# Optimization experiments

Hardware: AMD Instinct MI355X
Metric: run time of the kernel (lower is better)

The kernel has to match this reference:

```python
import jax, jax.numpy as jnp
import numpy as np

B, T, H, DK, DV, HID, C = 2, 4096, 16, 128, 128, 2048, 64  # chunk size 64 (fla default)
EPS = 1e-5


def setup_inputs() -> dict:
    key = jax.random.key(0)
    ks = jax.random.split(key, 8)
    s = 0.02
    return dict(
        hidden_ab=jax.random.normal(ks[0], (B, T, HID), jnp.float32),
        hidden_g=jax.random.normal(ks[1], (B, T, HID), jnp.float32),
        q=jax.random.normal(ks[2], (B, T, H, DK), jnp.float32),
        k=jax.random.normal(ks[3], (B, T, H, DK), jnp.float32),
        v=jax.random.normal(ks[4], (B, T, H, DV), jnp.float32),
        Wb=jax.random.normal(ks[5], (HID, H), jnp.float32) * s,
        Wg=jax.random.normal(ks[6], (HID, H), jnp.float32) * s,
        o_norm_w=jnp.ones((DV,), jnp.float32),
        o_proj_w=jax.random.normal(ks[7], (H, DV, DK), jnp.float32) * s,
    )


def _l2norm(x):
    return x * jax.lax.rsqrt(jnp.sum(x * x, -1, keepdims=True) + 1e-6)


def reference(hidden_ab, hidden_g, q, k, v, Wb, Wg, o_norm_w, o_proj_w):
    # beta gate per head (training path: sigmoid(b_proj(hidden_ab)))
    beta = jax.nn.sigmoid(hidden_ab @ Wb)  # [B,T,H]
    # qk_norm == 'l2' -> l2 normalization inside the kernel, q scaled by dk^-0.5
    q = _l2norm(q)
    k = _l2norm(k)
    scale = DK ** -0.5
    N = T // C

    def toc(x, d):  # [B,T,H,d] -> [N,B,H,C,d]
        return x.reshape(B, N, C, H, d).transpose(1, 0, 3, 2, 4)

    qc = toc(q * scale, DK)
    kc = toc(k, DK)
    vc = toc(v, DV)
    bc = beta.reshape(B, N, C, H).transpose(1, 0, 3, 2)  # [N,B,H,C]

    k_beta = kc * bc[..., None]
    v_beta = vc * bc[..., None]

    # intra-chunk UT transform: Tm = (I + strict_lower(k_beta k^T))^{-1}
    Lm = jnp.tril(jnp.einsum('nbhik,nbhjk->nbhij', k_beta, kc), -1)  # [N,B,H,C,C]
    eye = jnp.eye(C, dtype=q.dtype)
    Tm = jax.scipy.linalg.solve_triangular(eye + Lm, jnp.broadcast_to(eye, Lm.shape), lower=True)
    u = Tm @ v_beta   # [N,B,H,C,DV]
    w = Tm @ k_beta   # [N,B,H,C,DK]
    attn = jnp.tril(jnp.einsum('nbhik,nbhjk->nbhij', qc, kc))  # causal intra-chunk scores

    def step(S, ins):  # S: [B,H,DK,DV] carried state
        qn, kn, an, un, wn = ins
        vi = un - wn @ S                                   # corrected values
        on = qn @ S + an @ vi                              # inter + intra chunk output
        S = S + jnp.einsum('bhck,bhcv->bhkv', kn, vi)      # state update
        return S, on

    S0 = jnp.zeros((B, H, DK, DV), q.dtype)
    _, o = jax.lax.scan(step, S0, (qc, kc, attn, u, w))    # o: [N,B,H,C,DV]
    o = o.transpose(1, 0, 3, 2, 4).reshape(B, T, H, DV)

    # FusedRMSNormSwishGate with per-head scalar gate broadcast over DV
    g = hidden_g @ Wg  # [B,T,H]
    o = o * jax.lax.rsqrt(jnp.mean(o * o, -1, keepdims=True) + EPS) * o_norm_w
    o = o * (g * jax.nn.sigmoid(g))[..., None]

    # GroupLinear: per-head DV -> head_dim projection, then flatten heads
    out = jnp.einsum('bthv,hvd->bthd', o, o_proj_w).reshape(B, T, H * DK)
    return out
```

## Files before the change

kernel.cpp:

```cpp
#include <hip/hip_runtime.h>
#include <hip/hip_bf16.h>

#define BB 2
#define TT 4096
#define HH 16
#define DKk 128
#define DVv 128
#define HIDD 2048
#define CC 64
#define NN 64
#define GG 8
#define QSCALE 0.08838834764831845f

static __device__ __forceinline__ unsigned short f2bf(float f) {
  unsigned u = __float_as_uint(f);
  u += 0x7fffu + ((u >> 16) & 1u);
  return (unsigned short)(u >> 16);
}
static __device__ __forceinline__ float bf2f(unsigned short s) {
  return __uint_as_float(((unsigned)s) << 16);
}

static __device__ __forceinline__ void barrier_lds_only() {
  asm volatile("s_waitcnt lgkmcnt(0)\n\ts_barrier" ::: "memory");
}

typedef short bf8 __attribute__((ext_vector_type(8)));
typedef float f4 __attribute__((ext_vector_type(4)));

__global__ __launch_bounds__(256) void k0_wt(
    const float* __restrict__ Wb, const float* __restrict__ Wg,
    unsigned short* __restrict__ Wtb, unsigned short* __restrict__ Wtg) {
  int blk = blockIdx.x;
  const float* W = (blk < 8) ? Wb : Wg;
  unsigned short* Wt = (blk < 8) ? Wtb : Wtg;
  int k0 = (blk & 7) * 256;
  int tid = threadIdx.x;
  __shared__ unsigned short st[16][272];
  const float* p = W + (size_t)(k0 + tid) * HH;
#pragma unroll
  for (int h4 = 0; h4 < 4; h4++) {
    float4 x = *(const float4*)(p + h4 * 4);
    st[h4 * 4 + 0][tid] = f2bf(x.x);
    st[h4 * 4 + 1][tid] = f2bf(x.y);
    st[h4 * 4 + 2][tid] = f2bf(x.z);
    st[h4 * 4 + 3][tid] = f2bf(x.w);
  }
  __syncthreads();
  int h = tid >> 4, c = (tid & 15) << 4;
#pragma unroll
  for (int j = 0; j < 16; j++)
    Wt[(size_t)h * HIDD + k0 + c + j] = st[h][c + j];
}

__global__ __launch_bounds__(256) void k0p_pt(
    const float* __restrict__ opw, unsigned short* __restrict__ Ppt) {
  int h = blockIdx.x;
  int tid = threadIdx.x;
  __shared__ unsigned short sp[128 * 132];
  const float* P = opw + (size_t)h * (DVv * DKk);
  for (int it = 0; it < 16; it++) {
    int idx = it * 256 + tid;
    int vv = idx >> 5, d4 = (idx & 31) << 2;
    float4 x = *(const float4*)(P + vv * 128 + d4);
    sp[vv * 132 + d4 + 0] = f2bf(x.x);
    sp[vv * 132 + d4 + 1] = f2bf(x.y);
    sp[vv * 132 + d4 + 2] = f2bf(x.z);
    sp[vv * 132 + d4 + 3] = f2bf(x.w);
  }
  __syncthreads();
  unsigned short* dst = Ppt + (size_t)h * (DVv * DKk);
  for (int it = 0; it < 8; it++) {
    int idx = it * 256 + tid;
    int d = idx >> 4, v8 = (idx & 15) << 3;
    unsigned short tmp[8];
#pragma unroll
    for (int j = 0; j < 8; j++) tmp[j] = sp[(v8 + j) * 132 + d];
    *(uint4*)&dst[d * 128 + v8] = *(uint4*)tmp;
  }
}

__global__ __launch_bounds__(256) void k1_beta_g(
    const float* __restrict__ hab, const float* __restrict__ hg,
    const unsigned short* __restrict__ Wtb, const unsigned short* __restrict__ Wtg,
    float* __restrict__ beta, float* __restrict__ graw) {
  int tile = blockIdx.x;
  int tid = threadIdx.x;
  int w = tid >> 6, lane = tid & 63;
  int proj = w >> 1, ks = w & 1;
  int n16 = lane & 15, qd = lane >> 4;
  const float* hid = proj ? hg : hab;
  const unsigned short* Wt = proj ? Wtg : Wtb;
  size_t rowbase = (size_t)(tile * 16 + n16) * HIDD;
  int k0 = ks * 1024;

  f4 acc = {0.f, 0.f, 0.f, 0.f};
  for (int s = 0; s < 32; s++) {
    int kk = k0 + s * 32 + qd * 8;
    const float* hp = hid + rowbase + kk;
    float4 h0 = *(const float4*)hp;
    float4 h1 = *(const float4*)(hp + 4);
    bf8 a;
    a[0] = (short)f2bf(h0.x); a[1] = (short)f2bf(h0.y);
    a[2] = (short)f2bf(h0.z); a[3] = (short)f2bf(h0.w);
    a[4] = (short)f2bf(h1.x); a[5] = (short)f2bf(h1.y);
    a[6] = (short)f2bf(h1.z); a[7] = (short)f2bf(h1.w);
    bf8 b = *(const bf8*)&Wt[(size_t)n16 * HIDD + kk];
    acc = __builtin_amdgcn_mfma_f32_16x16x32_bf16(a, b, acc, 0, 0, 0);
  }

  __shared__ float red[2][16][17];
  if (ks == 1) {
#pragma unroll
    for (int r = 0; r < 4; r++) red[proj][qd * 4 + r][n16] = acc[r];
  }
  __syncthreads();
  if (ks == 0) {
#pragma unroll
    for (int r = 0; r < 4; r++) {
      float s = acc[r] + red[proj][qd * 4 + r][n16];
      size_t t = (size_t)(tile * 16 + qd * 4 + r) * HH + n16;
      if (proj == 0) beta[t] = 1.f / (1.f + expf(-s));
      else           graw[t] = s;
    }
  }
}

__global__ __launch_bounds__(256) void k2_l2norm(
    const float* __restrict__ q, const float* __restrict__ k,
    unsigned short* __restrict__ qn, unsigned short* __restrict__ kn) {
  int lane = threadIdx.x & 63, wave = threadIdx.x >> 6;
  for (int u = 0; u < 2; u++) {
    int vec = blockIdx.x * 8 + wave * 2 + u;
    size_t off = (size_t)vec * 64 + lane;
    float2 q2 = ((const float2*)q)[off];
    float2 k2 = ((const float2*)k)[off];
    float sq = q2.x * q2.x + q2.y * q2.y;
    float sk = k2.x * k2.x + k2.y * k2.y;
#pragma unroll
    for (int m = 32; m; m >>= 1) { sq += __shfl_xor(sq, m); sk += __shfl_xor(sk, m); }
    float rq = rsqrtf(sq + 1e-6f) * QSCALE;
    float rk = rsqrtf(sk + 1e-6f);
    unsigned pq = (unsigned)f2bf(q2.x * rq) | ((unsigned)f2bf(q2.y * rq) << 16);
    unsigned pk = (unsigned)f2bf(k2.x * rk) | ((unsigned)f2bf(k2.y * rk) << 16);
    ((unsigned*)qn)[off] = pq;
    ((unsigned*)kn)[off] = pk;
  }
}

#define SW 72
#define K3_M0R 8704
#define K3_M0T 13312
#define K3_M1R 17920
#define K3_M1T 22528
#define K3_TB  27136
#define K3_ARENA 31744

__global__ __launch_bounds__(256) void k3_chunk(
    const unsigned short* __restrict__ qn, const unsigned short* __restrict__ kn,
    const float* __restrict__ beta,
    unsigned short* __restrict__ ATg, unsigned short* __restrict__ Ktg) {
  int cid = blockIdx.x;
  int n = cid & (NN - 1);
  int bh = cid / NN;
  int h = bh & (HH - 1);
  int b = bh / HH;
  int tid = threadIdx.x;
  int w = tid >> 6;
  int lane = tid & 63;
  int n16 = lane & 15;
  int qd = lane >> 4;
  int r0 = w * 16;

  __shared__ __align__(16) unsigned short arena[K3_ARENA];
  __shared__ float sb[CC];
  unsigned short* sk = arena;
  unsigned short* sq = arena + 8704;

  int t0 = n * CC;
#pragma unroll
  for (int p = 0; p < 4; p++) {
    int id = p * 256 + tid, row = id >> 4, c8 = (id & 15) << 3;
    size_t g = ((size_t)((b * TT + t0 + row) * HH + h)) * DKk + c8;
    *(uint4*)&sk[row * 136 + c8] = *(const uint4*)(kn + g);
    *(uint4*)&sq[row * 136 + c8] = *(const uint4*)(qn + g);
  }
  if (tid < CC) sb[tid] = beta[(size_t)((b * TT + t0 + tid) * HH + h)];
  __syncthreads();

  f4 at[4], mk[4];
#pragma unroll
  for (int ct = 0; ct < 4; ct++) { at[ct] = (f4){0,0,0,0}; mk[ct] = (f4){0,0,0,0}; }
#pragma unroll
  for (int s = 0; s < 4; s++) {
    bf8 aq = *(const bf8*)&sq[(r0 + n16) * 136 + s * 32 + qd * 8];
    bf8 ak = *(const bf8*)&sk[(r0 + n16) * 136 + s * 32 + qd * 8];
#pragma unroll
    for (int ct = 0; ct < 4; ct++) {
      bf8 bk = *(const bf8*)&sk[(ct * 16 + n16) * 136 + s * 32 + qd * 8];
      at[ct] = __builtin_amdgcn_mfma_f32_16x16x32_bf16(aq, bk, at[ct], 0, 0, 0);
      mk[ct] = __builtin_amdgcn_mfma_f32_16x16x32_bf16(ak, bk, mk[ct], 0, 0, 0);
    }
  }

  f4 tf[4];
  float mpv[4][4];
#pragma unroll
  for (int ct = 0; ct < 4; ct++) {
#pragma unroll
    for (int r = 0; r < 4; r++) {
      int i = r0 + qd * 4 + r, j = ct * 16 + n16;
      at[ct][r] = (j <= i) ? at[ct][r] : 0.f;
      float mp = (j < i) ? -sb[i] * mk[ct][r] : 0.f;
      mpv[ct][r] = mp;
      tf[ct][r] = (i == j) ? 1.f : mp;
    }
  }
  __syncthreads();

#pragma unroll
  for (int ct = 0; ct < 4; ct++) {
#pragma unroll
    for (int r = 0; r < 4; r++) {
      int i = r0 + qd * 4 + r, j = ct * 16 + n16;
      unsigned short hm = f2bf(mpv[ct][r]);
      arena[K3_M0R + i * SW + j] = hm;
      arena[K3_M0T + j * SW + i] = hm;
      arena[K3_TB + j * SW + i] = f2bf(tf[ct][r]);
    }
  }
  __syncthreads();

  int p = 0;
  for (int it = 1; it <= 5; it++) {
    int mrp = p ? K3_M1R : K3_M0R, mtp = p ? K3_M1T : K3_M0T;
    int mrn = p ? K3_M0R : K3_M1R, mtn = p ? K3_M0T : K3_M1T;
    f4 nr[4];
#pragma unroll
    for (int ct = 0; ct < 4; ct++) nr[ct] = (f4){0,0,0,0};
#pragma unroll
    for (int s = 0; s < 2; s++) {
      bf8 a = *(const bf8*)&arena[mrp + (r0 + n16) * SW + s * 32 + qd * 8];
#pragma unroll
      for (int ct = 0; ct < 4; ct++) {
        bf8 bb = *(const bf8*)&arena[mtp + (ct * 16 + n16) * SW + s * 32 + qd * 8];
        nr[ct] = __builtin_amdgcn_mfma_f32_16x16x32_bf16(a, bb, nr[ct], 0, 0, 0);
      }
    }
#pragma unroll
    for (int ct = 0; ct < 4; ct++) {
#pragma unroll
      for (int r = 0; r < 4; r++) {
        int i = r0 + qd * 4 + r, j = ct * 16 + n16;
        unsigned short hm = f2bf(nr[ct][r]);
        arena[mrn + i * SW + j] = hm;
        arena[mtn + j * SW + i] = hm;
      }
    }
    __syncthreads();

#pragma unroll
    for (int s = 0; s < 2; s++) {
      bf8 a = *(const bf8*)&arena[mrn + (r0 + n16) * SW + s * 32 + qd * 8];
#pragma unroll
      for (int ct = 0; ct < 4; ct++) {
        bf8 bb = *(const bf8*)&arena[K3_TB + (ct * 16 + n16) * SW + s * 32 + qd * 8];
        tf[ct] = __builtin_amdgcn_mfma_f32_16x16x32_bf16(a, bb, tf[ct], 0, 0, 0);
      }
    }
    __syncthreads();

    if (it < 5) {
#pragma unroll
      for (int ct = 0; ct < 4; ct++) {
#pragma unroll
        for (int r = 0; r < 4; r++) {
          int i = r0 + qd * 4 + r, j = ct * 16 + n16;
          arena[K3_TB + j * SW + i] = f2bf(tf[ct][r]);
        }
      }
    }
    p = 1 - p;
  }

#pragma unroll
  for (int ct = 0; ct < 4; ct++) {
#pragma unroll
    for (int r = 0; r < 4; r++) {
      int i = r0 + qd * 4 + r, j = ct * 16 + n16;
      arena[K3_M0R + i * SW + j] = f2bf(at[ct][r]);
      arena[K3_TB + j * SW + i] = f2bf(tf[ct][r]);
    }
  }
  __syncthreads();

  {
    f4 ac[4];
#pragma unroll
    for (int ct = 0; ct < 4; ct++) ac[ct] = (f4){0,0,0,0};
#pragma unroll
    for (int s = 0; s < 2; s++) {
      bf8 a = *(const bf8*)&arena[K3_M0R + (r0 + n16) * SW + s * 32 + qd * 8];
#pragma unroll
      for (int ct = 0; ct < 4; ct++) {
        bf8 bb = *(const bf8*)&arena[K3_TB + (ct * 16 + n16) * SW + s * 32 + qd * 8];
        ac[ct] = __builtin_amdgcn_mfma_f32_16x16x32_bf16(a, bb, ac[ct], 0, 0, 0);
      }
    }
    size_t abase = (size_t)cid * (CC * CC);
#pragma unroll
    for (int ct = 0; ct < 4; ct++)
#pragma unroll
      for (int r = 0; r < 4; r++)
        ATg[abase + (r0 + qd * 4 + r) * CC + ct * 16 + n16] = f2bf(ac[ct][r]);
  }

  {
    size_t kbase = (size_t)cid * (DKk * CC);
#pragma unroll
    for (int t = 0; t < 2; t++) {
      int dkt = w * 32 + t * 16;
      f4 ac[4];
#pragma unroll
      for (int ct = 0; ct < 4; ct++) ac[ct] = (f4){0,0,0,0};
#pragma unroll
      for (int s = 0; s < 2; s++) {
        bf8 a;
#pragma unroll
        for (int jj = 0; jj < 8; jj++)
          a[jj] = (short)sk[(s * 32 + qd * 8 + jj) * 136 + dkt + n16];
#pragma unroll
        for (int ct = 0; ct < 4; ct++) {
          bf8 bb = *(const bf8*)&arena[K3_TB + (ct * 16 + n16) * SW + s * 32 + qd * 8];
          ac[ct] = __builtin_amdgcn_mfma_f32_16x16x32_bf16(a, bb, ac[ct], 0, 0, 0);
        }
      }
#pragma unroll
      for (int ct = 0; ct < 4; ct++)
#pragma unroll
        for (int r = 0; r < 4; r++)
          Ktg[kbase + (dkt + qd * 4 + r) * CC + ct * 16 + n16] = f2bf(ac[ct][r]);
    }
  }
}

struct K4Frag {
  bf8 k0, k1, k2, k3;
  bf8 q0, q1, q2, q3;
  bf8 a0, a1;
  bf8 t0, t1, t2, t3;
  float4 vv;
  float b0, b1, b2, b3;
};

static __device__ __forceinline__ void k4_prefetch(
    K4Frag& F, int n,
    const unsigned short* knb, const unsigned short* qnb,
    const unsigned short* atb, const unsigned short* ktb,
    const float* vb, const float* bb) {
  const unsigned short* kp = knb + (size_t)n * (CC * HH * DKk);
  F.k0 = *(const bf8*)(kp);
  F.k1 = *(const bf8*)(kp + 32);
  F.k2 = *(const bf8*)(kp + 64);
  F.k3 = *(const bf8*)(kp + 96);
  const unsigned short* qp = qnb + (size_t)n * (CC * HH * DKk);
  F.q0 = *(const bf8*)(qp);
  F.q1 = *(const bf8*)(qp + 32);
  F.q2 = *(const bf8*)(qp + 64);
  F.q3 = *(const bf8*)(qp + 96);
  const unsigned short* ap = atb + (size_t)n * (CC * CC);
  F.a0 = *(const bf8*)(ap);
  F.a1 = *(const bf8*)(ap + 32);
  const unsigned short* tp = ktb + (size_t)n * (DKk * CC);
  F.t0 = *(const bf8*)(tp);
  F.t1 = *(const bf8*)(tp + 32);
  F.t2 = *(const bf8*)(tp + 1024);
  F.t3 = *(const bf8*)(tp + 1024 + 32);
  F.vv = *(const float4*)(vb + (size_t)n * (CC * HH * DVv));
  const float* bp = bb + (size_t)n * (CC * HH);
  F.b0 = bp[0]; F.b1 = bp[HH]; F.b2 = bp[2 * HH]; F.b3 = bp[3 * HH];
}

static __device__ __forceinline__ void k4_body(
    const K4Frag& F, K4Frag& FN, int n, bool pf,
    f4& S0, f4& S1,
    unsigned short* xT, unsigned short* sSb,
    float* opn,
    int n16, int qd, int r0, int dkbase,
    const unsigned short* knb, const unsigned short* qnb,
    const unsigned short* atb, const unsigned short* ktb,
    const float* vb, const float* bb) {
  if (pf) k4_prefetch(FN, n + 1, knb, qnb, atb, ktb, vb, bb);

  {
    int col = r0 + n16;
    xT[(qd * 4 + 0) * SW + col] = f2bf(F.vv.x);
    xT[(qd * 4 + 1) * SW + col] = f2bf(F.vv.y);
    xT[(qd * 4 + 2) * SW + col] = f2bf(F.vv.z);
    xT[(qd * 4 + 3) * SW + col] = f2bf(F.vv.w);
  }
  barrier_lds_only();

  f4 oacc;
  {
    bf8 bS0 = *(const bf8*)&sSb[n16 * 136 + 0 + qd * 8];
    bf8 bS1 = *(const bf8*)&sSb[n16 * 136 + 32 + qd * 8];
    bf8 bS2 = *(const bf8*)&sSb[n16 * 136 + 64 + qd * 8];
    bf8 bS3 = *(const bf8*)&sSb[n16 * 136 + 96 + qd * 8];
    f4 xa = {0.f, 0.f, 0.f, 0.f}, xc = {0.f, 0.f, 0.f, 0.f};
    f4 oa = {0.f, 0.f, 0.f, 0.f}, ob = {0.f, 0.f, 0.f, 0.f};
    xa = __builtin_amdgcn_mfma_f32_16x16x32_bf16(F.k0, bS0, xa, 0, 0, 0);
    xa = __builtin_amdgcn_mfma_f32_16x16x32_bf16(F.k1, bS1, xa, 0, 0, 0);
    xc = __builtin_amdgcn_mfma_f32_16x16x32_bf16(F.k2, bS2, xc, 0, 0, 0);
    xc = __builtin_amdgcn_mfma_f32_16x16x32_bf16(F.k3, bS3, xc, 0, 0, 0);
    oa = __builtin_amdgcn_mfma_f32_16x16x32_bf16(F.q0, bS0, oa, 0, 0, 0);
    oa = __builtin_amdgcn_mfma_f32_16x16x32_bf16(F.q1, bS1, oa, 0, 0, 0);
    ob = __builtin_amdgcn_mfma_f32_16x16x32_bf16(F.q2, bS2, ob, 0, 0, 0);
    ob = __builtin_amdgcn_mfma_f32_16x16x32_bf16(F.q3, bS3, ob, 0, 0, 0);
    oacc = oa + ob;
    float bv[4] = {F.b0, F.b1, F.b2, F.b3};
#pragma unroll
    for (int r = 0; r < 4; r++) {
      int c = r0 + qd * 4 + r;
      float vval = bf2f(xT[n16 * SW + c]);
      xT[n16 * SW + c] = f2bf(bv[r] * (vval - (xa[r] + xc[r])));
    }
  }
  barrier_lds_only();

  {
    bf8 bx0 = *(const bf8*)&xT[n16 * SW + qd * 8];
    bf8 bx1 = *(const bf8*)&xT[n16 * SW + 32 + qd * 8];
    oacc = __builtin_amdgcn_mfma_f32_16x16x32_bf16(F.a0, bx0, oacc, 0, 0, 0);
    oacc = __builtin_amdgcn_mfma_f32_16x16x32_bf16(F.a1, bx1, oacc, 0, 0, 0);
#pragma unroll
    for (int r = 0; r < 4; r++) opn[r * (HH * DVv)] = oacc[r];
    S0 = __builtin_amdgcn_mfma_f32_16x16x32_bf16(F.t0, bx0, S0, 0, 0, 0);
    S0 = __builtin_amdgcn_mfma_f32_16x16x32_bf16(F.t1, bx1, S0, 0, 0, 0);
    S1 = __builtin_amdgcn_mfma_f32_16x16x32_bf16(F.t2, bx0, S1, 0, 0, 0);
    S1 = __builtin_amdgcn_mfma_f32_16x16x32_bf16(F.t3, bx1, S1, 0, 0, 0);
    uint2 w0, w1;
    w0.x = (unsigned)f2bf(S0[0]) | ((unsigned)f2bf(S0[1]) << 16);
    w0.y = (unsigned)f2bf(S0[2]) | ((unsigned)f2bf(S0[3]) << 16);
    w1.x = (unsigned)f2bf(S1[0]) | ((unsigned)f2bf(S1[1]) << 16);
    w1.y = (unsigned)f2bf(S1[2]) | ((unsigned)f2bf(S1[3]) << 16);
    *(uint2*)&sSb[n16 * 136 + dkbase + qd * 4] = w0;
    *(uint2*)&sSb[n16 * 136 + dkbase + 16 + qd * 4] = w1;
  }
}

__global__ __launch_bounds__(256, 1) void k4_scan(
    const unsigned short* __restrict__ qn, const unsigned short* __restrict__ kn,
    const float* __restrict__ v, const float* __restrict__ beta,
    const unsigned short* __restrict__ ATg, const unsigned short* __restrict__ Ktg,
    float* __restrict__ o) {
  int bi = blockIdx.x;
  int jg = bi >> 5;
  int bh = bi & 31;
  int h = bh & (HH - 1);
  int b = bh >> 4;
  int tid = threadIdx.x;
  int j0 = jg * 16;
  int w = tid >> 6;
  int lane = tid & 63;
  int n16 = lane & 15;
  int qd = lane >> 4;
  int r0 = w * 16;
  int dkbase = w * 32;

  __shared__ __align__(16) unsigned short sSb[16 * 136];
  __shared__ __align__(16) unsigned short sxT[2][16 * SW];

  f4 S0 = {0.f, 0.f, 0.f, 0.f}, S1 = {0.f, 0.f, 0.f, 0.f};
  for (int i = tid; i < 16 * 136; i += 256) sSb[i] = 0;

  const unsigned short* knb =
      kn + ((size_t)((b * TT + r0 + n16) * HH + h)) * DKk + qd * 8;
  const unsigned short* qnb =
      qn + ((size_t)((b * TT + r0 + n16) * HH + h)) * DKk + qd * 8;
  size_t bhN = (size_t)(b * HH + h) * NN;
  const unsigned short* atb = ATg + bhN * (CC * CC) + (r0 + n16) * 64 + qd * 8;
  const unsigned short* ktb = Ktg + bhN * (DKk * CC) + (dkbase + n16) * 64 + qd * 8;
  const float* vb =
      v + ((size_t)((b * TT + r0 + n16) * HH + h)) * DVv + j0 + qd * 4;
  const float* bb = beta + (size_t)((b * TT + r0 + qd * 4) * HH + h);
  float* opb =
      o + ((size_t)((b * TT + r0 + qd * 4) * HH + h)) * DVv + j0 + n16;

  K4Frag FA, FB;
  k4_prefetch(FA, 0, knb, qnb, atb, ktb, vb, bb);

  for (int n = 0; n < NN; n += 2) {
    k4_body(FA, FB, n, true, S0, S1, sxT[0], sSb,
            opb + (size_t)n * (CC * HH * DVv),
            n16, qd, r0, dkbase, knb, qnb, atb, ktb, vb, bb);
    k4_body(FB, FA, n + 1, n + 2 < NN, S0, S1, sxT[1], sSb,
            opb + (size_t)(n + 1) * (CC * HH * DVv),
            n16, qd, r0, dkbase, knb, qnb, atb, ktb, vb, bb);
  }
}

__global__ __launch_bounds__(256) void k5_out(
    const float* __restrict__ graw, const float* __restrict__ onw,
    const unsigned short* __restrict__ Ppt, float* __restrict__ out) {
  int bi = blockIdx.x;
  int h = bi & (HH - 1);
  int tt = (bi >> 4) & 127;
  int b = bi >> 11;
  int t0 = tt * 32;
  int tid = threadIdx.x;
  int w = tid >> 6;
  int lane = tid & 63;
  int n16 = lane & 15;
  int qd = lane >> 4;

  __shared__ __align__(16) float so[32 * 132];
  __shared__ float smul[32];
  __shared__ float snw[DVv];

  for (int r = 0; r < 16; r++) {
    int idx = r * 256 + tid;
    int t = idx >> 7, d = idx & 127;
    so[t * 132 + d] = out[((size_t)((b * TT + t0 + t) * HH + h)) * DVv + d];
  }
  if (tid < DVv) snw[tid] = onw[tid];
  __syncthreads();

  {
    int t = tid >> 3, l8 = tid & 7;
    float ss = 0.f;
    for (int j = 0; j < 16; j++) { float x = so[t * 132 + l8 + (j << 3)]; ss += x * x; }
    ss += __shfl_down(ss, 4, 8);
    ss += __shfl_down(ss, 2, 8);
    ss += __shfl_down(ss, 1, 8);
    if (l8 == 0) {
      float rms = rsqrtf(ss * (1.f / 128.f) + 1e-5f);
      float gv = graw[(size_t)((b * TT + t0 + t) * HH + h)];
      float sig = 1.f / (1.f + expf(-gv));
      smul[t] = rms * gv * sig;
    }
  }
  __syncthreads();
  for (int r = 0; r < 16; r++) {
    int idx = r * 256 + tid;
    int t = idx >> 7, d = idx & 127;
    so[t * 132 + d] *= smul[t] * snw[d];
  }
  __syncthreads();

  {
    const unsigned short* Pb = Ppt + (size_t)h * (DVv * DKk);
    int dt0 = w * 2;
#pragma unroll
    for (int m = 0; m < 2; m++) {
      bf8 A[4];
#pragma unroll
      for (int ks = 0; ks < 4; ks++) {
        const float* sp = &so[(m * 16 + n16) * 132 + ks * 32 + qd * 8];
        float4 f0 = *(const float4*)sp;
        float4 f1 = *(const float4*)(sp + 4);
        A[ks][0] = (short)f2bf(f0.x); A[ks][1] = (short)f2bf(f0.y);
        A[ks][2] = (short)f2bf(f0.z); A[ks][3] = (short)f2bf(f0.w);
        A[ks][4] = (short)f2bf(f1.x); A[ks][5] = (short)f2bf(f1.y);
        A[ks][6] = (short)f2bf(f1.z); A[ks][7] = (short)f2bf(f1.w);
      }
#pragma unroll
      for (int dti = 0; dti < 2; dti++) {
        int dt = dt0 + dti;
        f4 acc = {0.f, 0.f, 0.f, 0.f};
#pragma unroll
        for (int ks = 0; ks < 4; ks++) {
          bf8 Bf = *(const bf8*)(Pb + (dt * 16 + n16) * 128 + ks * 32 + qd * 8);
          acc = __builtin_amdgcn_mfma_f32_16x16x32_bf16(A[ks], Bf, acc, 0, 0, 0);
        }
#pragma unroll
        for (int r = 0; r < 4; r++) {
          size_t go = ((size_t)(b * TT + t0 + m * 16 + qd * 4 + r)) * (HH * DKk)
                      + h * DKk + dt * 16 + n16;
          out[go] = acc[r];
        }
      }
    }
  }
}

extern "C" void kernel_launch(void* const* d_in, const int* in_sizes, int n_in,
                              void* d_out, int out_size, void* d_ws, size_t ws_size,
                              hipStream_t stream) {
  (void)in_sizes; (void)n_in; (void)out_size; (void)ws_size;
  const float* hab = (const float*)d_in[0];
  const float* hg  = (const float*)d_in[1];
  const float* q   = (const float*)d_in[2];
  const float* k   = (const float*)d_in[3];
  const float* v   = (const float*)d_in[4];
  const float* Wb  = (const float*)d_in[5];
  const float* Wg  = (const float*)d_in[6];
  const float* onw = (const float*)d_in[7];
  const float* opw = (const float*)d_in[8];
  float* out = (float*)d_out;

  char* ws = (char*)d_ws;
  float* beta          = (float*)(ws);
  float* graw          = (float*)(ws + 524288);
  unsigned short* qn   = (unsigned short*)(ws + 1048576);
  unsigned short* kn   = (unsigned short*)(ws + 34603008);
  unsigned short* ATg  = (unsigned short*)(ws + 68157440);
  unsigned short* Ktg  = (unsigned short*)(ws + 84934656);
  unsigned short* Wtb  = (unsigned short*)(ws + 118489088);
  unsigned short* Wtg  = (unsigned short*)(ws + 118554624);
  unsigned short* Ppt  = (unsigned short*)(ws + 118620160);

  hipLaunchKernelGGL(k0_wt, dim3(16), dim3(256), 0, stream,
                     Wb, Wg, Wtb, Wtg);
  hipLaunchKernelGGL(k0p_pt, dim3(HH), dim3(256), 0, stream,
                     opw, Ppt);
  hipLaunchKernelGGL(k1_beta_g, dim3(TT * BB / 16), dim3(256), 0, stream,
                     hab, hg, Wtb, Wtg, beta, graw);
  hipLaunchKernelGGL(k2_l2norm, dim3(BB * TT * HH / 8), dim3(256), 0, stream,
                     q, k, qn, kn);
  hipLaunchKernelGGL(k3_chunk, dim3(BB * HH * NN), dim3(256), 0, stream,
                     qn, kn, beta, ATg, Ktg);
  hipLaunchKernelGGL(k4_scan, dim3(BB * HH * GG), dim3(256), 0, stream,
                     qn, kn, v, beta, ATg, Ktg, out);
  hipLaunchKernelGGL(k5_out, dim3(BB * (TT / 32) * HH), dim3(256), 0, stream,
                     graw, onw, Ppt, out);
}
```

Measured before the change: 533.6 us.

## Restructure scan: precompute beta-scaled k and v, double-buffer state to drop a barrier

Two new precomputed inputs feed the sequential scan. A beta-scaled bf16 key is written alongside qn/kn, and a new kernel writes beta-scaled, transposed bf16 values that reuse the kn buffer once k3 has finished with it. The scan stages the shared beta-k tile in double-buffered LDS and double-buffers the state, so each chunk step needs one barrier instead of two, and it uses packed bf16 conversion instructions. The cost is an extra pre-pass kernel, more global traffic and more LDS, with ordering that depends on k3 finishing before vt overwrites kn.

```diff
diff --git a/kernel.cpp b/kernel.cpp
--- a/kernel.cpp
+++ b/kernel.cpp
@@ -20,13 +20,26 @@
 static __device__ __forceinline__ float bf2f(unsigned short s) {
   return __uint_as_float(((unsigned)s) << 16);
 }
+static __device__ __forceinline__ unsigned cvtpk(float lo, float hi) {
+  unsigned r;
+  asm("v_cvt_pk_bf16_f32 %0, %1, %2" : "=v"(r) : "v"(lo), "v"(hi));
+  return r;
+}
 
 static __device__ __forceinline__ void barrier_lds_only() {
   asm volatile("s_waitcnt lgkmcnt(0)\n\ts_barrier" ::: "memory");
 }
 
 typedef short bf8 __attribute__((ext_vector_type(8)));
+typedef short bf4 __attribute__((ext_vector_type(4)));
 typedef float f4 __attribute__((ext_vector_type(4)));
+
+static __device__ __forceinline__ bf4 pack_bf4(float a, float b, float c, float d) {
+  union { uint2 u; bf4 s; } t;
+  t.u.x = cvtpk(a, b);
+  t.u.y = cvtpk(c, d);
+  return t.s;
+}
 
 __global__ __launch_bounds__(256) void k0_wt(
     const float* __restrict__ Wb, const float* __restrict__ Wg,
@@ -128,23 +141,68 @@
 
 __global__ __launch_bounds__(256) void k2_l2norm(
     const float* __restrict__ q, const float* __restrict__ k,
-    unsigned short* __restrict__ qn, unsigned short* __restrict__ kn) {
+    const float* __restrict__ beta,
+    unsigned short* __restrict__ qn, unsigned short* __restrict__ kn,
+    unsigned short* __restrict__ kb) {
   int lane = threadIdx.x & 63, wave = threadIdx.x >> 6;
   for (int u = 0; u < 2; u++) {
     int vec = blockIdx.x * 8 + wave * 2 + u;
     size_t off = (size_t)vec * 64 + lane;
     float2 q2 = ((const float2*)q)[off];
     float2 k2 = ((const float2*)k)[off];
+    float bv = beta[vec];
     float sq = q2.x * q2.x + q2.y * q2.y;
     float sk = k2.x * k2.x + k2.y * k2.y;
 #pragma unroll
     for (int m = 32; m; m >>= 1) { sq += __shfl_xor(sq, m); sk += __shfl_xor(sk, m); }
     float rq = rsqrtf(sq + 1e-6f) * QSCALE;
     float rk = rsqrtf(sk + 1e-6f);
+    float rkb = rk * bv;
     unsigned pq = (unsigned)f2bf(q2.x * rq) | ((unsigned)f2bf(q2.y * rq) << 16);
     unsigned pk = (unsigned)f2bf(k2.x * rk) | ((unsigned)f2bf(k2.y * rk) << 16);
+    unsigned pb = (unsigned)f2bf(k2.x * rkb) | ((unsigned)f2bf(k2.y * rkb) << 16);
     ((unsigned*)qn)[off] = pq;
     ((unsigned*)kn)[off] = pk;
+    ((unsigned*)kb)[off] = pb;
+  }
+}
+
+__global__ __launch_bounds__(256) void k2v_vt(
+    const float* __restrict__ v, const float* __restrict__ beta,
+    unsigned short* __restrict__ vt) {
+  int bi = blockIdx.x;
+  int n = bi & (NN - 1);
+  int bh = bi >> 6;
+  int h = bh & (HH - 1);
+  int b = bh >> 4;
+  int tid = threadIdx.x;
+  int t0 = n * CC;
+
+  __shared__ float sov[64 * 132];
+  __shared__ float sbv[64];
+
+  for (int p = 0; p < 8; p++) {
+    int idx = p * 256 + tid;
+    int row = idx >> 5, d4 = (idx & 31) << 2;
+    float4 x = *(const float4*)(v + ((size_t)((b * TT + t0 + row) * HH + h)) * DVv + d4);
+    *(float4*)&sov[row * 132 + d4] = x;
+  }
+  if (tid < 64) sbv[tid] = beta[(size_t)((b * TT + t0 + tid) * HH + h)];
+  __syncthreads();
+
+  unsigned short* dst = vt + (size_t)(bh * NN + n) * 8192;
+  for (int p = 0; p < 8; p++) {
+    int q = p * 256 + tid;
+    int rt = q >> 9, col = (q >> 2) & 127, i4 = q & 3;
+    int m = rt * 16 + i4 * 4;
+    float x0 = sbv[m + 0] * sov[(m + 0) * 132 + col];
+    float x1 = sbv[m + 1] * sov[(m + 1) * 132 + col];
+    float x2 = sbv[m + 2] * sov[(m + 2) * 132 + col];
+    float x3 = sbv[m + 3] * sov[(m + 3) * 132 + col];
+    uint2 wv;
+    wv.x = cvtpk(x0, x1);
+    wv.y = cvtpk(x2, x3);
+    *(uint2*)&dst[(size_t)q * 4] = wv;
   }
 }
 
@@ -344,25 +402,17 @@
   }
 }
 
-struct K4Frag {
-  bf8 k0, k1, k2, k3;
+struct K4F {
   bf8 q0, q1, q2, q3;
   bf8 a0, a1;
   bf8 t0, t1, t2, t3;
-  float4 vv;
-  float b0, b1, b2, b3;
+  uint2 v0, v1, v2, v3;
 };
 
-static __device__ __forceinline__ void k4_prefetch(
-    K4Frag& F, int n,
-    const unsigned short* knb, const unsigned short* qnb,
-    const unsigned short* atb, const unsigned short* ktb,
-    const float* vb, const float* bb) {
-  const unsigned short* kp = knb + (size_t)n * (CC * HH * DKk);
-  F.k0 = *(const bf8*)(kp);
-  F.k1 = *(const bf8*)(kp + 32);
-  F.k2 = *(const bf8*)(kp + 64);
-  F.k3 = *(const bf8*)(kp + 96);
+static __device__ __forceinline__ void k4_pref(
+    K4F& F, int n,
+    const unsigned short* qnb, const unsigned short* atb,
+    const unsigned short* ktb, const unsigned short* vtb) {
   const unsigned short* qp = qnb + (size_t)n * (CC * HH * DKk);
   F.q0 = *(const bf8*)(qp);
   F.q1 = *(const bf8*)(qp + 32);
@@ -375,83 +425,102 @@
   F.t0 = *(const bf8*)(tp);
   F.t1 = *(const bf8*)(tp + 32);
   F.t2 = *(const bf8*)(tp + 1024);
-  F.t3 = *(const bf8*)(tp + 1024 + 32);
-  F.vv = *(const float4*)(vb + (size_t)n * (CC * HH * DVv));
-  const float* bp = bb + (size_t)n * (CC * HH);
-  F.b0 = bp[0]; F.b1 = bp[HH]; F.b2 = bp[2 * HH]; F.b3 = bp[3 * HH];
+  F.t3 = *(const bf8*)(tp + 1056);
+  const unsigned short* vp = vtb + (size_t)n * 8192;
+  F.v0 = *(const uint2*)(vp);
+  F.v1 = *(const uint2*)(vp + 2048);
+  F.v2 = *(const uint2*)(vp + 4096);
+  F.v3 = *(const uint2*)(vp + 6144);
 }
 
 static __device__ __forceinline__ void k4_body(
-    const K4Frag& F, K4Frag& FN, int n, bool pf,
-    f4& S0, f4& S1,
-    unsigned short* xT, unsigned short* sSb,
-    float* opn,
-    int n16, int qd, int r0, int dkbase,
-    const unsigned short* knb, const unsigned short* qnb,
-    const unsigned short* atb, const unsigned short* ktb,
-    const float* vb, const float* bb) {
-  if (pf) k4_prefetch(FN, n + 1, knb, qnb, atb, ktb, vb, bb);
-
+    const K4F& F, K4F& FN, int n,
+    f4& S0, f4& S1, uint4* KB,
+    const unsigned short* sSrd, unsigned short* sSwr,
+    const unsigned short* kbRd, unsigned short* kbWr,
+    unsigned short* xbw, float* opn,
+    int tid, int lane, int n16, int qd, int dkbase,
+    const unsigned short* qnb, const unsigned short* atb,
+    const unsigned short* ktb, const unsigned short* vtb,
+    const unsigned short* kbg, const size_t* gkb) {
+  if (n + 1 < NN) {
+#pragma unroll
+    for (int p = 0; p < 4; p++)
+      *(uint4*)&kbWr[(size_t)(p * 256 + tid) * 8] = KB[p];
+  }
+  if (n + 2 < NN) {
+#pragma unroll
+    for (int p = 0; p < 4; p++)
+      KB[p] = *(const uint4*)(kbg + gkb[p] + (size_t)(n + 2) * (CC * HH * DKk));
+  }
+  if (n + 1 < NN) k4_pref(FN, n + 1, qnb, atb, ktb, vtb);
+
+  bf8 bS0 = *(const bf8*)&sSrd[n16 * 136 + 0  + qd * 8];
+  bf8 bS1 = *(const bf8*)&sSrd[n16 * 136 + 32 + qd * 8];
+  bf8 bS2 = *(const bf8*)&sSrd[n16 * 136 + 64 + qd * 8];
+  bf8 bS3 = *(const bf8*)&sSrd[n16 * 136 + 96 + qd * 8];
+
+  f4 oa = {0.f, 0.f, 0.f, 0.f}, ob = {0.f, 0.f, 0.f, 0.f};
+  oa = __builtin_amdgcn_mfma_f32_16x16x32_bf16(F.q0, bS0, oa, 0, 0, 0);
+  oa = __builtin_amdgcn_mfma_f32_16x16x32_bf16(F.q1, bS1, oa, 0, 0, 0);
+  ob = __builtin_amdgcn_mfma_f32_16x16x32_bf16(F.q2, bS2, ob, 0, 0, 0);
+  ob = __builtin_amdgcn_mfma_f32_16x16x32_bf16(F.q3, bS3, ob, 0, 0, 0);
+
+  f4 xlo[4], xhi[4];
+#pragma unroll
+  for (int rt = 0; rt < 4; rt++) {
+    bf8 kf0 = *(const bf8*)&kbRd[(size_t)((rt * 4 + 0) * 64 + lane) * 8];
+    bf8 kf1 = *(const bf8*)&kbRd[(size_t)((rt * 4 + 1) * 64 + lane) * 8];
+    bf8 kf2 = *(const bf8*)&kbRd[(size_t)((rt * 4 + 2) * 64 + lane) * 8];
+    bf8 kf3 = *(const bf8*)&kbRd[(size_t)((rt * 4 + 3) * 64 + lane) * 8];
+    f4 lo = {0.f, 0.f, 0.f, 0.f}, hi = {0.f, 0.f, 0.f, 0.f};
+    lo = __builtin_amdgcn_mfma_f32_16x16x32_bf16(kf0, bS0, lo, 0, 0, 0);
+    lo = __builtin_amdgcn_mfma_f32_16x16x32_bf16(kf1, bS1, lo, 0, 0, 0);
+    hi = __builtin_amdgcn_mfma_f32_16x16x32_bf16(kf2, bS2, hi, 0, 0, 0);
+    hi = __builtin_amdgcn_mfma_f32_16x16x32_bf16(kf3, bS3, hi, 0, 0, 0);
+    xlo[rt] = lo;
+    xhi[rt] = hi;
+  }
   {
-    int col = r0 + n16;
-    xT[(qd * 4 + 0) * SW + col] = f2bf(F.vv.x);
-    xT[(qd * 4 + 1) * SW + col] = f2bf(F.vv.y);
-    xT[(qd * 4 + 2) * SW + col] = f2bf(F.vv.z);
-    xT[(qd * 4 + 3) * SW + col] = f2bf(F.vv.w);
-  }
+    const uint2 vv[4] = {F.v0, F.v1, F.v2, F.v3};
+#pragma unroll
+    for (int rt = 0; rt < 4; rt++) {
+      float w0 = bf2f((unsigned short)(vv[rt].x & 0xffffu));
+      float w1 = bf2f((unsigned short)(vv[rt].x >> 16));
+      float w2 = bf2f((unsigned short)(vv[rt].y & 0xffffu));
+      float w3 = bf2f((unsigned short)(vv[rt].y >> 16));
+      bf4 pw = pack_bf4(w0 - (xlo[rt][0] + xhi[rt][0]),
+                        w1 - (xlo[rt][1] + xhi[rt][1]),
+                        w2 - (xlo[rt][2] + xhi[rt][2]),
+                        w3 - (xlo[rt][3] + xhi[rt][3]));
+      *(bf4*)&xbw[n16 * 88 + rt * 16 + qd * 4] = pw;
+    }
+  }
+  bf8 bx0 = *(const bf8*)&xbw[n16 * 88 + 0  + qd * 8];
+  bf8 bx1 = *(const bf8*)&xbw[n16 * 88 + 32 + qd * 8];
+
+  f4 oacc = oa + ob;
+  oacc = __builtin_amdgcn_mfma_f32_16x16x32_bf16(F.a0, bx0, oacc, 0, 0, 0);
+  oacc = __builtin_amdgcn_mfma_f32_16x16x32_bf16(F.a1, bx1, oacc, 0, 0, 0);
+#pragma unroll
+  for (int r = 0; r < 4; r++) opn[r * (HH * DVv)] = oacc[r];
+
+  S0 = __builtin_amdgcn_mfma_f32_16x16x32_bf16(F.t0, bx0, S0, 0, 0, 0);
+  S0 = __builtin_amdgcn_mfma_f32_16x16x32_bf16(F.t1, bx1, S0, 0, 0, 0);
+  S1 = __builtin_amdgcn_mfma_f32_16x16x32_bf16(F.t2, bx0, S1, 0, 0, 0);
+  S1 = __builtin_amdgcn_mfma_f32_16x16x32_bf16(F.t3, bx1, S1, 0, 0, 0);
+
+  *(bf4*)&sSwr[n16 * 136 + dkbase + qd * 4] =
+      pack_bf4(S0[0], S0[1], S0[2], S0[3]);
+  *(bf4*)&sSwr[n16 * 136 + dkbase + 16 + qd * 4] =
+      pack_bf4(S1[0], S1[1], S1[2], S1[3]);
+
   barrier_lds_only();
-
-  f4 oacc;
-  {
-    bf8 bS0 = *(const bf8*)&sSb[n16 * 136 + 0 + qd * 8];
-    bf8 bS1 = *(const bf8*)&sSb[n16 * 136 + 32 + qd * 8];
-    bf8 bS2 = *(const bf8*)&sSb[n16 * 136 + 64 + qd * 8];
-    bf8 bS3 = *(const bf8*)&sSb[n16 * 136 + 96 + qd * 8];
-    f4 xa = {0.f, 0.f, 0.f, 0.f}, xc = {0.f, 0.f, 0.f, 0.f};
-    f4 oa = {0.f, 0.f, 0.f, 0.f}, ob = {0.f, 0.f, 0.f, 0.f};
-    xa = __builtin_amdgcn_mfma_f32_16x16x32_bf16(F.k0, bS0, xa, 0, 0, 0);
-    xa = __builtin_amdgcn_mfma_f32_16x16x32_bf16(F.k1, bS1, xa, 0, 0, 0);
-    xc = __builtin_amdgcn_mfma_f32_16x16x32_bf16(F.k2, bS2, xc, 0, 0, 0);
-    xc = __builtin_amdgcn_mfma_f32_16x16x32_bf16(F.k3, bS3, xc, 0, 0, 0);
-    oa = __builtin_amdgcn_mfma_f32_16x16x32_bf16(F.q0, bS0, oa, 0, 0, 0);
-    oa = __builtin_amdgcn_mfma_f32_16x16x32_bf16(F.q1, bS1, oa, 0, 0, 0);
-    ob = __builtin_amdgcn_mfma_f32_16x16x32_bf16(F.q2, bS2, ob, 0, 0, 0);
-    ob = __builtin_amdgcn_mfma_f32_16x16x32_bf16(F.q3, bS3, ob, 0, 0, 0);
-    oacc = oa + ob;
-    float bv[4] = {F.b0, F.b1, F.b2, F.b3};
-#pragma unroll
-    for (int r = 0; r < 4; r++) {
-      int c = r0 + qd * 4 + r;
-      float vval = bf2f(xT[n16 * SW + c]);
-      xT[n16 * SW + c] = f2bf(bv[r] * (vval - (xa[r] + xc[r])));
-    }
-  }
-  barrier_lds_only();
-
-  {
-    bf8 bx0 = *(const bf8*)&xT[n16 * SW + qd * 8];
-    bf8 bx1 = *(const bf8*)&xT[n16 * SW + 32 + qd * 8];
-    oacc = __builtin_amdgcn_mfma_f32_16x16x32_bf16(F.a0, bx0, oacc, 0, 0, 0);
-    oacc = __builtin_amdgcn_mfma_f32_16x16x32_bf16(F.a1, bx1, oacc, 0, 0, 0);
-#pragma unroll
-    for (int r = 0; r < 4; r++) opn[r * (HH * DVv)] = oacc[r];
-    S0 = __builtin_amdgcn_mfma_f32_16x16x32_bf16(F.t0, bx0, S0, 0, 0, 0);
-    S0 = __builtin_amdgcn_mfma_f32_16x16x32_bf16(F.t1, bx1, S0, 0, 0, 0);
-    S1 = __builtin_amdgcn_mfma_f32_16x16x32_bf16(F.t2, bx0, S1, 0, 0, 0);
-    S1 = __builtin_amdgcn_mfma_f32_16x16x32_bf16(F.t3, bx1, S1, 0, 0, 0);
-    uint2 w0, w1;
-    w0.x = (unsigned)f2bf(S0[0]) | ((unsigned)f2bf(S0[1]) << 16);
-    w0.y = (unsigned)f2bf(S0[2]) | ((unsigned)f2bf(S0[3]) << 16);
-    w1.x = (unsigned)f2bf(S1[0]) | ((unsigned)f2bf(S1[1]) << 16);
-    w1.y = (unsigned)f2bf(S1[2]) | ((unsigned)f2bf(S1[3]) << 16);
-    *(uint2*)&sSb[n16 * 136 + dkbase + qd * 4] = w0;
-    *(uint2*)&sSb[n16 * 136 + dkbase + 16 + qd * 4] = w1;
-  }
 }
 
 __global__ __launch_bounds__(256, 1) void k4_scan(
-    const unsigned short* __restrict__ qn, const unsigned short* __restrict__ kn,
-    const float* __restrict__ v, const float* __restrict__ beta,
+    const unsigned short* __restrict__ qn, const unsigned short* __restrict__ kb,
+    const unsigned short* __restrict__ vt,
     const unsigned short* __restrict__ ATg, const unsigned short* __restrict__ Ktg,
     float* __restrict__ o) {
   int bi = blockIdx.x;
@@ -468,35 +537,49 @@
   int r0 = w * 16;
   int dkbase = w * 32;
 
-  __shared__ __align__(16) unsigned short sSb[16 * 136];
-  __shared__ __align__(16) unsigned short sxT[2][16 * SW];
+  __shared__ __align__(16) unsigned short sSb[2][16 * 136];
+  __shared__ __align__(16) unsigned short kbL[2][CC * DKk];
+  __shared__ __align__(16) unsigned short xbuf[4][16 * 88];
 
   f4 S0 = {0.f, 0.f, 0.f, 0.f}, S1 = {0.f, 0.f, 0.f, 0.f};
-  for (int i = tid; i < 16 * 136; i += 256) sSb[i] = 0;
-
-  const unsigned short* knb =
-      kn + ((size_t)((b * TT + r0 + n16) * HH + h)) * DKk + qd * 8;
+  for (int i = tid; i < 2 * 16 * 136; i += 256) ((unsigned short*)sSb)[i] = 0;
+
   const unsigned short* qnb =
       qn + ((size_t)((b * TT + r0 + n16) * HH + h)) * DKk + qd * 8;
   size_t bhN = (size_t)(b * HH + h) * NN;
   const unsigned short* atb = ATg + bhN * (CC * CC) + (r0 + n16) * 64 + qd * 8;
   const unsigned short* ktb = Ktg + bhN * (DKk * CC) + (dkbase + n16) * 64 + qd * 8;
-  const float* vb =
-      v + ((size_t)((b * TT + r0 + n16) * HH + h)) * DVv + j0 + qd * 4;
-  const float* bb = beta + (size_t)((b * TT + r0 + qd * 4) * HH + h);
+  const unsigned short* vtb = vt + bhN * 8192 + (size_t)(j0 + n16) * 16 + qd * 4;
   float* opb =
       o + ((size_t)((b * TT + r0 + qd * 4) * HH + h)) * DVv + j0 + n16;
 
-  K4Frag FA, FB;
-  k4_prefetch(FA, 0, knb, qnb, atb, ktb, vb, bb);
+  size_t gkb[4];
+#pragma unroll
+  for (int p = 0; p < 4; p++)
+    gkb[p] = ((size_t)((b * TT + p * 16 + n16) * HH + h)) * DKk + w * 32 + qd * 8;
+
+  uint4 KB[4];
+  K4F FA, FB;
+  unsigned short* xbw = xbuf[w];
+
+#pragma unroll
+  for (int p = 0; p < 4; p++) KB[p] = *(const uint4*)(kb + gkb[p]);
+#pragma unroll
+  for (int p = 0; p < 4; p++)
+    *(uint4*)&kbL[0][(size_t)(p * 256 + tid) * 8] = KB[p];
+#pragma unroll
+  for (int p = 0; p < 4; p++)
+    KB[p] = *(const uint4*)(kb + gkb[p] + (size_t)(CC * HH * DKk));
+  k4_pref(FA, 0, qnb, atb, ktb, vtb);
+  __syncthreads();
 
   for (int n = 0; n < NN; n += 2) {
-    k4_body(FA, FB, n, true, S0, S1, sxT[0], sSb,
-            opb + (size_t)n * (CC * HH * DVv),
-            n16, qd, r0, dkbase, knb, qnb, atb, ktb, vb, bb);
-    k4_body(FB, FA, n + 1, n + 2 < NN, S0, S1, sxT[1], sSb,
-            opb + (size_t)(n + 1) * (CC * HH * DVv),
-            n16, qd, r0, dkbase, knb, qnb, atb, ktb, vb, bb);
+    k4_body(FA, FB, n, S0, S1, KB, sSb[0], sSb[1], kbL[0], kbL[1],
+            xbw, opb + (size_t)n * (CC * HH * DVv),
+            tid, lane, n16, qd, dkbase, qnb, atb, ktb, vtb, kb, gkb);
+    k4_body(FB, FA, n + 1, S0, S1, KB, sSb[1], sSb[0], kbL[1], kbL[0],
+            xbw, opb + (size_t)(n + 1) * (CC * HH * DVv),
+            tid, lane, n16, qd, dkbase, qnb, atb, ktb, vtb, kb, gkb);
   }
 }
 
@@ -604,11 +687,13 @@
   float* graw          = (float*)(ws + 524288);
   unsigned short* qn   = (unsigned short*)(ws + 1048576);
   unsigned short* kn   = (unsigned short*)(ws + 34603008);
+  unsigned short* vt   = kn;
   unsigned short* ATg  = (unsigned short*)(ws + 68157440);
   unsigned short* Ktg  = (unsigned short*)(ws + 84934656);
   unsigned short* Wtb  = (unsigned short*)(ws + 118489088);
   unsigned short* Wtg  = (unsigned short*)(ws + 118554624);
   unsigned short* Ppt  = (unsigned short*)(ws + 118620160);
+  unsigned short* kb   = (unsigned short*)(ws + 119144448);
 
   hipLaunchKernelGGL(k0_wt, dim3(16), dim3(256), 0, stream,
                      Wb, Wg, Wtb, Wtg);
@@ -617,11 +702,13 @@
   hipLaunchKernelGGL(k1_beta_g, dim3(TT * BB / 16), dim3(256), 0, stream,
                      hab, hg, Wtb, Wtg, beta, graw);
   hipLaunchKernelGGL(k2_l2norm, dim3(BB * TT * HH / 8), dim3(256), 0, stream,
-                     q, k, qn, kn);
+                     q, k, beta, qn, kn, kb);
   hipLaunchKernelGGL(k3_chunk, dim3(BB * HH * NN), dim3(256), 0, stream,
                      qn, kn, beta, ATg, Ktg);
+  hipLaunchKernelGGL(k2v_vt, dim3(BB * HH * NN), dim3(256), 0, stream,
+                     v, beta, vt);
   hipLaunchKernelGGL(k4_scan, dim3(BB * HH * GG), dim3(256), 0, stream,
-                     qn, kn, v, beta, ATg, Ktg, out);
+                     qn, kb, vt, ATg, Ktg, out);
   hipLaunchKernelGGL(k5_out, dim3(BB * (TT / 32) * HH), dim3(256), 0, stream,
                      graw, onw, Ppt, out);
 }
```

New measurement: 624.4 us. +17.0%, slower.

## Split scan value columns into overlapping 16-wide windows owning 8 columns each

Applied to the files above, without the earlier changes.

The chunked recurrence kernel now launches 16 groups per (batch, head) instead of 8. Each block still computes a 16-column DV tile (the MFMA width), but each owns only 8 output columns, with the last window shifted to stay in range. Only the owned lanes write output. This doubles the block count and sets launch bounds to 2 blocks per CU to improve occupancy on the latency-bound serial scan, at the cost of computing every state column twice. LDS reads and writes are also vectorised into 4-element bf16 packs.

```diff
diff --git a/kernel.cpp b/kernel.cpp
--- a/kernel.cpp
+++ b/kernel.cpp
@@ -9,7 +9,7 @@
 #define HIDD 2048
 #define CC 64
 #define NN 64
-#define GG 8
+#define GGS 16
 #define QSCALE 0.08838834764831845f
 
 static __device__ __forceinline__ unsigned short f2bf(float f) {
@@ -26,7 +26,15 @@
 }
 
 typedef short bf8 __attribute__((ext_vector_type(8)));
+typedef short bf4 __attribute__((ext_vector_type(4)));
 typedef float f4 __attribute__((ext_vector_type(4)));
+
+static __device__ __forceinline__ bf4 pack_bf4(float a, float b, float c, float d) {
+  bf4 r;
+  r[0] = (short)f2bf(a); r[1] = (short)f2bf(b);
+  r[2] = (short)f2bf(c); r[3] = (short)f2bf(d);
+  return r;
+}
 
 __global__ __launch_bounds__(256) void k0_wt(
     const float* __restrict__ Wb, const float* __restrict__ Wg,
@@ -382,7 +390,7 @@
 }
 
 static __device__ __forceinline__ void k4_body(
-    const K4Frag& F, K4Frag& FN, int n, bool pf,
+    const K4Frag& F, K4Frag& FN, int n, bool pf, bool ostore,
     f4& S0, f4& S1,
     unsigned short* xT, unsigned short* sSb,
     float* opn,
@@ -418,13 +426,13 @@
     ob = __builtin_amdgcn_mfma_f32_16x16x32_bf16(F.q2, bS2, ob, 0, 0, 0);
     ob = __builtin_amdgcn_mfma_f32_16x16x32_bf16(F.q3, bS3, ob, 0, 0, 0);
     oacc = oa + ob;
+    bf4 vv4 = *(const bf4*)&xT[n16 * SW + r0 + qd * 4];
     float bv[4] = {F.b0, F.b1, F.b2, F.b3};
-#pragma unroll
-    for (int r = 0; r < 4; r++) {
-      int c = r0 + qd * 4 + r;
-      float vval = bf2f(xT[n16 * SW + c]);
-      xT[n16 * SW + c] = f2bf(bv[r] * (vval - (xa[r] + xc[r])));
-    }
+    float xr[4];
+#pragma unroll
+    for (int r = 0; r < 4; r++)
+      xr[r] = bv[r] * (bf2f((unsigned short)vv4[r]) - (xa[r] + xc[r]));
+    *(bf4*)&xT[n16 * SW + r0 + qd * 4] = pack_bf4(xr[0], xr[1], xr[2], xr[3]);
   }
   barrier_lds_only();
 
@@ -433,23 +441,20 @@
     bf8 bx1 = *(const bf8*)&xT[n16 * SW + 32 + qd * 8];
     oacc = __builtin_amdgcn_mfma_f32_16x16x32_bf16(F.a0, bx0, oacc, 0, 0, 0);
     oacc = __builtin_amdgcn_mfma_f32_16x16x32_bf16(F.a1, bx1, oacc, 0, 0, 0);
-#pragma unroll
-    for (int r = 0; r < 4; r++) opn[r * (HH * DVv)] = oacc[r];
+    if (ostore) {
+#pragma unroll
+      for (int r = 0; r < 4; r++) opn[r * (HH * DVv)] = oacc[r];
+    }
     S0 = __builtin_amdgcn_mfma_f32_16x16x32_bf16(F.t0, bx0, S0, 0, 0, 0);
     S0 = __builtin_amdgcn_mfma_f32_16x16x32_bf16(F.t1, bx1, S0, 0, 0, 0);
     S1 = __builtin_amdgcn_mfma_f32_16x16x32_bf16(F.t2, bx0, S1, 0, 0, 0);
     S1 = __builtin_amdgcn_mfma_f32_16x16x32_bf16(F.t3, bx1, S1, 0, 0, 0);
-    uint2 w0, w1;
-    w0.x = (unsigned)f2bf(S0[0]) | ((unsigned)f2bf(S0[1]) << 16);
-    w0.y = (unsigned)f2bf(S0[2]) | ((unsigned)f2bf(S0[3]) << 16);
-    w1.x = (unsigned)f2bf(S1[0]) | ((unsigned)f2bf(S1[1]) << 16);
-    w1.y = (unsigned)f2bf(S1[2]) | ((unsigned)f2bf(S1[3]) << 16);
-    *(uint2*)&sSb[n16 * 136 + dkbase + qd * 4] = w0;
-    *(uint2*)&sSb[n16 * 136 + dkbase + 16 + qd * 4] = w1;
-  }
-}
-
-__global__ __launch_bounds__(256, 1) void k4_scan(
+    *(bf4*)&sSb[n16 * 136 + dkbase + qd * 4] = pack_bf4(S0[0], S0[1], S0[2], S0[3]);
+    *(bf4*)&sSb[n16 * 136 + dkbase + 16 + qd * 4] = pack_bf4(S1[0], S1[1], S1[2], S1[3]);
+  }
+}
+
+__global__ __launch_bounds__(256, 2) void k4_scan(
     const unsigned short* __restrict__ qn, const unsigned short* __restrict__ kn,
     const float* __restrict__ v, const float* __restrict__ beta,
     const unsigned short* __restrict__ ATg, const unsigned short* __restrict__ Ktg,
@@ -460,13 +465,16 @@
   int h = bh & (HH - 1);
   int b = bh >> 4;
   int tid = threadIdx.x;
-  int j0 = jg * 16;
+  int j0w = jg * 8;
+  int jw = (jg == 15) ? 112 : jg * 8;
+  int lo = j0w - jw;
   int w = tid >> 6;
   int lane = tid & 63;
   int n16 = lane & 15;
   int qd = lane >> 4;
   int r0 = w * 16;
   int dkbase = w * 32;
+  bool ostore = ((unsigned)(n16 - lo)) < 8u;
 
   __shared__ __align__(16) unsigned short sSb[16 * 136];
   __shared__ __align__(16) unsigned short sxT[2][16 * SW];
@@ -482,19 +490,19 @@
   const unsigned short* atb = ATg + bhN * (CC * CC) + (r0 + n16) * 64 + qd * 8;
   const unsigned short* ktb = Ktg + bhN * (DKk * CC) + (dkbase + n16) * 64 + qd * 8;
   const float* vb =
-      v + ((size_t)((b * TT + r0 + n16) * HH + h)) * DVv + j0 + qd * 4;
+      v + ((size_t)((b * TT + r0 + n16) * HH + h)) * DVv + jw + qd * 4;
   const float* bb = beta + (size_t)((b * TT + r0 + qd * 4) * HH + h);
   float* opb =
-      o + ((size_t)((b * TT + r0 + qd * 4) * HH + h)) * DVv + j0 + n16;
+      o + ((size_t)((b * TT + r0 + qd * 4) * HH + h)) * DVv + jw + n16;
 
   K4Frag FA, FB;
   k4_prefetch(FA, 0, knb, qnb, atb, ktb, vb, bb);
 
   for (int n = 0; n < NN; n += 2) {
-    k4_body(FA, FB, n, true, S0, S1, sxT[0], sSb,
+    k4_body(FA, FB, n, true, ostore, S0, S1, sxT[0], sSb,
             opb + (size_t)n * (CC * HH * DVv),
             n16, qd, r0, dkbase, knb, qnb, atb, ktb, vb, bb);
-    k4_body(FB, FA, n + 1, n + 2 < NN, S0, S1, sxT[1], sSb,
+    k4_body(FB, FA, n + 1, n + 2 < NN, ostore, S0, S1, sxT[1], sSb,
             opb + (size_t)(n + 1) * (CC * HH * DVv),
             n16, qd, r0, dkbase, knb, qnb, atb, ktb, vb, bb);
   }
@@ -620,7 +628,7 @@
                      q, k, qn, kn);
   hipLaunchKernelGGL(k3_chunk, dim3(BB * HH * NN), dim3(256), 0, stream,
                      qn, kn, beta, ATg, Ktg);
-  hipLaunchKernelGGL(k4_scan, dim3(BB * HH * GG), dim3(256), 0, stream,
+  hipLaunchKernelGGL(k4_scan, dim3(BB * HH * GGS), dim3(256), 0, stream,
                      qn, kn, v, beta, ATg, Ktg, out);
   hipLaunchKernelGGL(k5_out, dim3(BB * (TT / 32) * HH), dim3(256), 0, stream,
                      graw, onw, Ppt, out);
```

Result: slower. 649.8 us (+21.8%).
